# Optimization experiments

Hardware: AMD Instinct MI355X
Metric: run time of the kernel (lower is better)

## Reference

```python
import jax, jax.numpy as jnp
import numpy as np

B, L, H, NHEADS = 32, 1024, 128, 2
HEAD = H // NHEADS
NEG = -2.0**32 + 1.0  # padding value used by the torch module


def setup_inputs() -> dict:
    key = jax.random.key(0)
    ks = jax.random.split(key, 9)
    queries = jax.random.normal(ks[0], (B, L, H), dtype=jnp.float32)
    keys = jax.random.normal(ks[1], (B, L, H), dtype=jnp.float32)
    time_mask = jax.random.bernoulli(ks[2], 0.1, (B, L))
    # causal mask: True above the diagonal (future positions masked)
    attn_mask = jnp.triu(jnp.ones((L, L), dtype=bool), k=1)
    s = 1.0 / np.sqrt(H)
    Qw = jax.random.uniform(ks[3], (H, H), jnp.float32, -s, s)
    Qb = jax.random.uniform(ks[4], (H,), jnp.float32, -s, s)
    Kw = jax.random.uniform(ks[5], (H, H), jnp.float32, -s, s)
    Kb = jax.random.uniform(ks[6], (H,), jnp.float32, -s, s)
    Vw = jax.random.uniform(ks[7], (H, H), jnp.float32, -s, s)
    Vb = jax.random.uniform(ks[8], (H,), jnp.float32, -s, s)
    return {"queries": queries, "keys": keys, "time_mask": time_mask,
            "attn_mask": attn_mask, "Qw": Qw, "Qb": Qb, "Kw": Kw, "Kb": Kb,
            "Vw": Vw, "Vb": Vb}


def reference(queries, keys, time_mask, attn_mask, Qw, Qb, Kw, Kb, Vw, Vb):
    b, l, h = queries.shape
    d = h // NHEADS
    # torch Linear: x @ W.T + b
    Q = queries @ Qw.T + Qb
    K = keys @ Kw.T + Kb
    V = keys @ Vw.T + Vb
    # split heads: torch cat(split(dim=2), dim=0) == (h, B, L, d) layout;
    # equivalent per-head math with (B, h, L, d):
    Qh = Q.reshape(b, l, NHEADS, d).transpose(0, 2, 1, 3)  # bhld
    Kh = K.reshape(b, l, NHEADS, d).transpose(0, 2, 1, 3)
    Vh = V.reshape(b, l, NHEADS, d).transpose(0, 2, 1, 3)
    scores = jnp.einsum('bhqd,bhkd->bhqk', Qh, Kh) / jnp.sqrt(
        jnp.asarray(d, dtype=Qh.dtype))
    # time_mask masks whole query rows; attn_mask is causal over (q, k)
    scores = jnp.where(time_mask[:, None, :, None], NEG, scores)
    scores = jnp.where(attn_mask[None, None, :, :], NEG, scores)
    attn = jax.nn.softmax(scores, axis=-1)  # dropout_rate=0 -> identity
    out = jnp.einsum('bhqk,bhkd->bhqd', attn, Vh)
    return out.transpose(0, 2, 1, 3).reshape(b, l, h)
```

## Files before the change

kernel.cpp:

```cpp
#include <hip/hip_runtime.h>

#define LSEQ 1024
#define DH 64
#define NH 2

typedef __attribute__((ext_vector_type(8))) __bf16 bf16x8;
typedef __attribute__((ext_vector_type(4))) float f32x4;
typedef __attribute__((ext_vector_type(16))) float f32x16;
typedef __attribute__((ext_vector_type(4))) unsigned u32x4;
typedef __attribute__((ext_vector_type(8))) unsigned short ushort8;

__device__ __forceinline__ unsigned short f2bf(float f) {
  unsigned u = __float_as_uint(f);
  u += 0x7FFFu + ((u >> 16) & 1u);
  return (unsigned short)(u >> 16);
}
__device__ __forceinline__ unsigned cvt_pk_bf16(float lo, float hi) {
  unsigned r;
  asm("v_cvt_pk_bf16_f32 %0, %1, %2" : "=v"(r) : "v"(lo), "v"(hi));
  return r;
}
__device__ __forceinline__ void gload16(const void* g, void* l) {
  __builtin_amdgcn_global_load_lds(
      (const __attribute__((address_space(1))) void*)g,
      (__attribute__((address_space(3))) void*)l, 16, 0, 0);
}

#define QSCALE 0.1803368801111601f

__global__ __launch_bounds__(256) void wconv_kernel(
    const float* __restrict__ Qw, const float* __restrict__ Kw,
    const float* __restrict__ Vw, unsigned short* __restrict__ Wbf,
    float* __restrict__ Vmean)
{
  const int t = blockIdx.x * 256 + threadIdx.x;
  if (t < NH * 32 * DH) Vmean[t] = 0.f;
  const int m = t >> 12;
  const float* W = (m == 0) ? Qw : (m == 1) ? Kw : Vw;
  const float4 v = ((const float4*)W)[t & 4095];
  uint2 u;
  u.x = cvt_pk_bf16(v.x, v.y);
  u.y = cvt_pk_bf16(v.z, v.w);
  *(uint2*)&Wbf[t * 4] = u;
}

__global__ __launch_bounds__(256, 3) void proj_kernel(
    const float* __restrict__ queries, const float* __restrict__ keys,
    const unsigned short* __restrict__ Wbf,
    const float* __restrict__ Qb, const float* __restrict__ Kb,
    const float* __restrict__ Vb,
    unsigned short* __restrict__ Qbf, unsigned short* __restrict__ Kbf,
    unsigned short* __restrict__ Vt, float* __restrict__ Vmean)
{
  constexpr int LP = 136;
  __shared__ __align__(16) unsigned short Xs[128 * LP];
  __shared__ __align__(16) unsigned short Wh[8192];

  const int t = threadIdx.x;
  const int lane = t & 63, w = t >> 6;
  const int c = lane & 15, g = lane >> 4;
  const int wrow = w * 32;

  const int mat = blockIdx.x >> 8;
  const int rt  = (blockIdx.x & 255) * 128;
  const float* Xin = (mat == 0) ? queries : keys;
  const char* Wg = (const char*)(Wbf + mat * 16384);

#define WSTAGE_H(h) do {                                                   \
    _Pragma("unroll")                                                      \
    for (int i_ = 0; i_ < 4; ++i_) {                                       \
      const int off_ = t * 16 + i_ * 4096;                   \
      const int lrow_ = off_ >> 7;                             \
      const int lch_ = (off_ >> 4) & 7;                                    \
      gload16(Wg + lrow_ * 256 + (h) * 128 + ((lch_ ^ (lrow_ & 7)) << 4),  \
              (char*)Wh + off_);                                           \
    }                                                                      \
  } while (0)

#define WFRAG_H(ct_, j_) \
  (*(const bf16x8*)&Wh[((ct_) * 16 + c) * 64 + (((j_) ^ (c & 7)) << 3)])

#define XFRAG(half_, kc_) \
  (*(const bf16x8*)&Xs[(wrow + (half_) * 16 + c) * LP + (kc_) * 32 + g * 8])

  WSTAGE_H(0);

  const float4* X4 = (const float4*)(Xin + (size_t)rt * 128);
#pragma unroll
  for (int i = 0; i < 16; ++i) {
    const int e4 = t + i * 256;
    const float4 v = X4[e4];
    const int e = e4 * 4;
    uint2 u;
    u.x = cvt_pk_bf16(v.x, v.y);
    u.y = cvt_pk_bf16(v.z, v.w);
    *(uint2*)&Xs[(e >> 7) * LP + (e & 127)] = u;
  }
  __syncthreads();

  f32x4 acc[2][8];
#pragma unroll
  for (int i = 0; i < 2; ++i)
#pragma unroll
    for (int j = 0; j < 8; ++j) acc[i][j] = (f32x4){0.f, 0.f, 0.f, 0.f};

#pragma unroll
  for (int kc2 = 0; kc2 < 2; ++kc2) {
    const bf16x8 a0 = XFRAG(0, kc2);
    const bf16x8 a1 = XFRAG(1, kc2);
#pragma unroll
    for (int ct = 0; ct < 8; ++ct) {
      const bf16x8 bfr = WFRAG_H(ct, kc2 * 4 + g);
      acc[0][ct] = __builtin_amdgcn_mfma_f32_16x16x32_bf16(a0, bfr, acc[0][ct], 0, 0, 0);
      acc[1][ct] = __builtin_amdgcn_mfma_f32_16x16x32_bf16(a1, bfr, acc[1][ct], 0, 0, 0);
    }
  }
  __syncthreads();
  WSTAGE_H(1);
  __syncthreads();

#pragma unroll
  for (int kc2 = 0; kc2 < 2; ++kc2) {
    const bf16x8 a0 = XFRAG(0, kc2 + 2);
    const bf16x8 a1 = XFRAG(1, kc2 + 2);
#pragma unroll
    for (int ct = 0; ct < 8; ++ct) {
      const bf16x8 bfr = WFRAG_H(ct, kc2 * 4 + g);
      acc[0][ct] = __builtin_amdgcn_mfma_f32_16x16x32_bf16(a0, bfr, acc[0][ct], 0, 0, 0);
      acc[1][ct] = __builtin_amdgcn_mfma_f32_16x16x32_bf16(a1, bfr, acc[1][ct], 0, 0, 0);
    }
  }

  if (mat == 2) {
#pragma unroll
    for (int ct = 0; ct < 8; ++ct) {
      const float bv = Vb[ct * 16 + c];
      float cs = 8.f * bv;
#pragma unroll
      for (int qf = 0; qf < 2; ++qf)
#pragma unroll
        for (int r = 0; r < 4; ++r) cs += acc[qf][ct][r];
      cs += __shfl_xor(cs, 16);
      cs += __shfl_xor(cs, 32);
      if (g == 0) {
        const int col = ct * 16 + c;
        const int bh = (rt >> 10) * NH + (col >> 6);
        atomicAdd(&Vmean[bh * DH + (col & 63)], cs);
      }
    }
    __syncthreads();
#pragma unroll
    for (int qf = 0; qf < 2; ++qf)
#pragma unroll
      for (int ct = 0; ct < 8; ++ct) {
        const float bv = Vb[ct * 16 + c];
        const int col = ct * 16 + c;
        uint2 u;
        u.x = cvt_pk_bf16(acc[qf][ct][0] + bv, acc[qf][ct][1] + bv);
        u.y = cvt_pk_bf16(acc[qf][ct][2] + bv, acc[qf][ct][3] + bv);
        *(uint2*)&Xs[col * LP + wrow + qf * 16 + g * 4] = u;
      }
    __syncthreads();
    const int b = rt >> 10, l0 = rt & 1023;
#pragma unroll
    for (int i = 0; i < 8; ++i) {
      const int e = i * 2048 + t * 8;
      const int col = e >> 7, li = e & 127;
      const ushort8 v8 = *(const ushort8*)&Xs[col * LP + li];
      const int hh = col >> 6, dh = col & 63;
      unsigned short* vp = Vt + ((size_t)(b * NH + hh)) * (DH * LSEQ) +
                           (size_t)dh * LSEQ + l0 + li;
      *(ushort8*)vp = v8;
    }
  } else {
    const float* biasA = mat ? Kb : Qb;
    const float qs = mat ? 1.0f : QSCALE;
    __syncthreads();
#pragma unroll
    for (int qf = 0; qf < 2; ++qf)
#pragma unroll
      for (int ct = 0; ct < 8; ++ct) {
        const float bv = biasA[ct * 16 + c];
#pragma unroll
        for (int r = 0; r < 4; ++r)
          Xs[(wrow + qf * 16 + g * 4 + r) * LP + ct * 16 + c] =
              f2bf((acc[qf][ct][r] + bv) * qs);
      }
    __syncthreads();
    unsigned short* outp = (mat ? Kbf : Qbf) + (size_t)rt * 128;
#pragma unroll
    for (int i = 0; i < 8; ++i) {
      const int e = i * 2048 + t * 8;
      *(ushort8*)&outp[e] = *(const ushort8*)&Xs[(e >> 7) * LP + (e & 127)];
    }
  }
#undef WSTAGE_H
#undef WFRAG_H
#undef XFRAG
}

__global__ __launch_bounds__(128, 2) void attn_kernel(
    const unsigned short* __restrict__ Qbf, const unsigned short* __restrict__ Kbf,
    const unsigned short* __restrict__ Vt, const float* __restrict__ Vmean,
    const int* __restrict__ time_mask, float* __restrict__ out)
{
  __shared__ __align__(16) char smem[33280];

  const int tid = threadIdx.x;
  const int lane = tid & 63, w = tid >> 6;
  const int lq = lane & 31, hi = lane >> 5;
  const int s7 = lq & 7;

  const int wgid = blockIdx.x;
  const int xcd = wgid & 7;
  const int idx = wgid >> 3;
  const int bh  = xcd * 8 + (idx & 7);
  const int qt  = 15 - (idx >> 3);
  const int qbase = qt * 64;
  const int b = bh >> 1, h = bh & 1;

  const unsigned short* Qp = Qbf + ((size_t)b * LSEQ) * 128 + h * 64;
  const char* Kpb = (const char*)(Kbf + ((size_t)b * LSEQ) * 128 + h * 64);
  const char* Vpb = (const char*)(Vt + (size_t)bh * (DH * LSEQ));

  const int nkv = qt + 1;

#define STAGE(tkv, bi) do {                                                   \
    const int kv_ = (tkv) * 64;                                               \
    _Pragma("unroll")                                                         \
    for (int r_ = 0; r_ < 4; ++r_) {                                          \
      const int off_ = tid * 16 + r_ * 2048;                                  \
      const int row_ = off_ >> 7;                                             \
      const int chk_ = (((off_ >> 4) & 7) ^ (row_ & 7)) << 4;                 \
      gload16(Kpb + (size_t)(kv_ + row_) * 256 + chk_,                        \
              (char*)smem + (bi) * 8192 + r_ * 2048 + tid * 16);              \
      gload16(Vpb + (size_t)row_ * 2048 + kv_ * 2 + chk_,                     \
              (char*)smem + 16384 + (bi) * 8192 + r_ * 2048 + tid * 16);      \
    }                                                                         \
  } while (0)

#define PLSWAP(x_, y_) asm("v_permlane32_swap_b32 %0, %1" : "+v"(x_), "+v"(y_))

#define MKPA(pk_, m_, dst_) do {                                              \
    unsigned x0_ = pk_[4*(m_)], x1_ = pk_[4*(m_)+1];                          \
    unsigned y0_ = pk_[4*(m_)+2], y1_ = pk_[4*(m_)+3];                        \
    PLSWAP(x0_, y0_); PLSWAP(x1_, y1_);                                       \
    u32x4 u_ = {x0_, x1_, y0_, y1_};                                          \
    dst_ = *(bf16x8*)&u_;                                                     \
  } while (0)

  bf16x8 qa[4];
#pragma unroll
  for (int kc4 = 0; kc4 < 4; ++kc4)
    qa[kc4] = *(const bf16x8*)&Qp[(qbase + w * 32 + lq) * 128 + kc4 * 16 + hi * 8];

  const __bf16 one = (__bf16)1.0f;
  const bf16x8 vones = {one, one, one, one, one, one, one, one};

  f32x16 acc0 = {}, acc1 = {}, acc5 = {};

  STAGE(0, 0);
  __syncthreads();

  for (int tk = 0; tk < nkv; ++tk) {
    const int cur = tk & 1;
    if (tk + 1 < nkv) STAGE(tk + 1, cur ^ 1);

    const char* Kl = smem + cur * 8192;
    const char* Vl = smem + 16384 + cur * 8192;

    f32x16 s0 = {}, s1 = {};
    __builtin_amdgcn_s_setprio(1);
#pragma unroll
    for (int kc4 = 0; kc4 < 4; ++kc4) {
      const bf16x8 kf = *(const bf16x8*)(Kl + (lq << 7) + (((2 * kc4 + hi) ^ s7) << 4));
      s0 = __builtin_amdgcn_mfma_f32_32x32x16_bf16(kf, qa[kc4], s0, 0, 0, 0);
    }
#pragma unroll
    for (int kc4 = 0; kc4 < 4; ++kc4) {
      const bf16x8 kf = *(const bf16x8*)(Kl + ((32 + lq) << 7) + (((2 * kc4 + hi) ^ s7) << 4));
      s1 = __builtin_amdgcn_mfma_f32_32x32x16_bf16(kf, qa[kc4], s1, 0, 0, 0);
    }
    __builtin_amdgcn_s_setprio(0);

    bf16x8 vf[4][2];
#pragma unroll
    for (int kc4 = 0; kc4 < 4; ++kc4)
#pragma unroll
      for (int dt = 0; dt < 2; ++dt)
        vf[kc4][dt] = *(const bf16x8*)(Vl + ((dt * 32 + lq) << 7) + (((2 * kc4 + hi) ^ s7) << 4));

    const bool diag = (tk == nkv - 1);
    const int kv = tk * 64;
    const int qrow = qbase + w * 32 + lq;
    float p0[16], p1[16];
#pragma unroll
    for (int r = 0; r < 16; ++r) {
      const int krow = (r & 3) + 8 * (r >> 2) + 4 * hi;
      float e0 = __builtin_amdgcn_exp2f(s0[r]);
      float e1 = __builtin_amdgcn_exp2f(s1[r]);
      if (diag) {
        if (kv + krow > qrow)      e0 = 0.f;
        if (kv + 32 + krow > qrow) e1 = 0.f;
      }
      p0[r] = e0; p1[r] = e1;
    }

    unsigned pk0[8], pk1[8];
#pragma unroll
    for (int bb = 0; bb < 4; ++bb) {
      pk0[2*bb]   = cvt_pk_bf16(p0[4*bb],   p0[4*bb+1]);
      pk0[2*bb+1] = cvt_pk_bf16(p0[4*bb+2], p0[4*bb+3]);
      pk1[2*bb]   = cvt_pk_bf16(p1[4*bb],   p1[4*bb+1]);
      pk1[2*bb+1] = cvt_pk_bf16(p1[4*bb+2], p1[4*bb+3]);
    }

    bf16x8 pa;
    __builtin_amdgcn_s_setprio(1);
    MKPA(pk0, 0, pa);
    acc0 = __builtin_amdgcn_mfma_f32_32x32x16_bf16(pa, vf[0][0], acc0, 0, 0, 0);
    acc1 = __builtin_amdgcn_mfma_f32_32x32x16_bf16(pa, vf[0][1], acc1, 0, 0, 0);
    acc5 = __builtin_amdgcn_mfma_f32_32x32x16_bf16(pa, vones,    acc5, 0, 0, 0);
    MKPA(pk0, 1, pa);
    acc0 = __builtin_amdgcn_mfma_f32_32x32x16_bf16(pa, vf[1][0], acc0, 0, 0, 0);
    acc1 = __builtin_amdgcn_mfma_f32_32x32x16_bf16(pa, vf[1][1], acc1, 0, 0, 0);
    acc5 = __builtin_amdgcn_mfma_f32_32x32x16_bf16(pa, vones,    acc5, 0, 0, 0);
    MKPA(pk1, 0, pa);
    acc0 = __builtin_amdgcn_mfma_f32_32x32x16_bf16(pa, vf[2][0], acc0, 0, 0, 0);
    acc1 = __builtin_amdgcn_mfma_f32_32x32x16_bf16(pa, vf[2][1], acc1, 0, 0, 0);
    acc5 = __builtin_amdgcn_mfma_f32_32x32x16_bf16(pa, vones,    acc5, 0, 0, 0);
    MKPA(pk1, 1, pa);
    acc0 = __builtin_amdgcn_mfma_f32_32x32x16_bf16(pa, vf[3][0], acc0, 0, 0, 0);
    acc1 = __builtin_amdgcn_mfma_f32_32x32x16_bf16(pa, vf[3][1], acc1, 0, 0, 0);
    acc5 = __builtin_amdgcn_mfma_f32_32x32x16_bf16(pa, vones,    acc5, 0, 0, 0);
    __builtin_amdgcn_s_setprio(0);

    __syncthreads();
  }

  int* tmx = (int*)(smem + 32768 + w * 128);
  if (hi == 0)
    tmx[lq] = time_mask[b * LSEQ + qbase + w * 32 + lq];
  asm volatile("s_waitcnt lgkmcnt(0)" ::: "memory");
  __builtin_amdgcn_sched_barrier(0);

  const float vmv0 = Vmean[bh * DH + lq]      * (1.0f / 1024.0f);
  const float vmv1 = Vmean[bh * DH + 32 + lq] * (1.0f / 1024.0f);

#pragma unroll
  for (int r = 0; r < 16; ++r) {
    const int qr = (r & 3) + 8 * (r >> 2) + 4 * hi;
    const int tm = tmx[qr];
    const float wv = 1.0f / acc5[r];
    float* orow = out + (size_t)(b * LSEQ + qbase + w * 32 + qr) * (NH * DH) + h * DH;
    orow[lq]      = tm ? vmv0 : acc0[r] * wv;
    orow[32 + lq] = tm ? vmv1 : acc1[r] * wv;
  }
#undef STAGE
#undef PLSWAP
#undef MKPA
}

extern "C" void kernel_launch(void* const* d_in, const int* in_sizes, int n_in,
                              void* d_out, int out_size, void* d_ws, size_t ws_size,
                              hipStream_t stream) {
  const float* queries   = (const float*)d_in[0];
  const float* keys      = (const float*)d_in[1];
  const int*   time_mask = (const int*)d_in[2];
  const float* Qw = (const float*)d_in[4];
  const float* Qb = (const float*)d_in[5];
  const float* Kw = (const float*)d_in[6];
  const float* Kb = (const float*)d_in[7];
  const float* Vw = (const float*)d_in[8];
  const float* Vb = (const float*)d_in[9];
  float* out = (float*)d_out;

  char* ws = (char*)d_ws;
  unsigned short* Wbf   = (unsigned short*)(ws);
  float*          Vmean = (float*)(ws + 98304);
  unsigned short* Qbf   = (unsigned short*)(ws + 114688);
  unsigned short* Kbf   = (unsigned short*)(ws + 8503296);
  unsigned short* Vtp   = (unsigned short*)(ws + 16891904);

  wconv_kernel<<<48, 256, 0, stream>>>(Qw, Kw, Vw, Wbf, Vmean);
  proj_kernel<<<768, 256, 0, stream>>>(queries, keys, Wbf, Qb, Kb, Vb,
                                       Qbf, Kbf, Vtp, Vmean);
  attn_kernel<<<1024, 128, 0, stream>>>(Qbf, Kbf, Vtp, Vmean, time_mask, out);
}
```

Measured before the change: 46.29 us.

## Balance causal attention work by splitting upper query tiles across workgroups with atomics

Restructures the attention grid to balance causal work. Half the workgroups compute the upper-half query tiles over the key tiles from 8 up to the diagonal, then also run a full lower-half query tile. The other half compute the upper-half query tiles over key tiles 0–7 and add partial numerators and row sums into the output with atomics. A new normalization kernel divides the upper-half rows by the accumulated sums and applies the time mask. The weight-conversion kernel gains extra blocks that zero the accumulation targets. This evens out per-workgroup work, at the cost of float atomics, an extra launch, and an extra pass over half the output.

```diff
diff --git a/kernel.cpp b/kernel.cpp
--- a/kernel.cpp
+++ b/kernel.cpp
@@ -31,17 +31,32 @@
 __global__ __launch_bounds__(256) void wconv_kernel(
     const float* __restrict__ Qw, const float* __restrict__ Kw,
     const float* __restrict__ Vw, unsigned short* __restrict__ Wbf,
-    float* __restrict__ Vmean)
+    float* __restrict__ Vmean, float* __restrict__ out,
+    float* __restrict__ lsumbuf)
 {
-  const int t = blockIdx.x * 256 + threadIdx.x;
-  if (t < NH * 32 * DH) Vmean[t] = 0.f;
-  const int m = t >> 12;
-  const float* W = (m == 0) ? Qw : (m == 1) ? Kw : Vw;
-  const float4 v = ((const float4*)W)[t & 4095];
-  uint2 u;
-  u.x = cvt_pk_bf16(v.x, v.y);
-  u.y = cvt_pk_bf16(v.z, v.w);
-  *(uint2*)&Wbf[t * 4] = u;
+  if (blockIdx.x < 48) {
+    const int t = blockIdx.x * 256 + threadIdx.x;
+    if (t < NH * 32 * DH) Vmean[t] = 0.f;
+    const int m = t >> 12;
+    const float* W = (m == 0) ? Qw : (m == 1) ? Kw : Vw;
+    const float4 v = ((const float4*)W)[t & 4095];
+    uint2 u;
+    u.x = cvt_pk_bf16(v.x, v.y);
+    u.y = cvt_pk_bf16(v.z, v.w);
+    *(uint2*)&Wbf[t * 4] = u;
+  } else {
+    const int gid = (blockIdx.x - 48) * 256 + threadIdx.x;
+    const float4 z = {0.f, 0.f, 0.f, 0.f};
+    const int f4 = gid * 2;
+    const int bb = f4 >> 14;
+    const int rem = f4 & 16383;
+    float4* p = (float4*)(out + (size_t)bb * 131072 + 65536) + rem;
+    p[0] = z; p[1] = z;
+    if (gid < 8192) {
+      float4* q = (float4*)lsumbuf + gid * 2;
+      q[0] = z; q[1] = z;
+    }
+  }
 }
 
 __global__ __launch_bounds__(256, 3) void proj_kernel(
@@ -202,7 +217,8 @@
 __global__ __launch_bounds__(128, 2) void attn_kernel(
     const unsigned short* __restrict__ Qbf, const unsigned short* __restrict__ Kbf,
     const unsigned short* __restrict__ Vt, const float* __restrict__ Vmean,
-    const int* __restrict__ time_mask, float* __restrict__ out)
+    const int* __restrict__ time_mask, float* __restrict__ out,
+    float* __restrict__ lsumbuf)
 {
   __shared__ __align__(16) char smem[33280];
 
@@ -215,15 +231,22 @@
   const int xcd = wgid & 7;
   const int idx = wgid >> 3;
   const int bh  = xcd * 8 + (idx & 7);
-  const int qt  = 15 - (idx >> 3);
-  const int qbase = qt * 64;
+  const int ucode = idx >> 3;
   const int b = bh >> 1, h = bh & 1;
 
   const unsigned short* Qp = Qbf + ((size_t)b * LSEQ) * 128 + h * 64;
   const char* Kpb = (const char*)(Kbf + ((size_t)b * LSEQ) * 128 + h * 64);
   const char* Vpb = (const char*)(Vt + (size_t)bh * (DH * LSEQ));
 
-  const int nkv = qt + 1;
+  const int comb = (ucode < 8);
+  int qbase, tkb, tke, tdiag, part;
+  const int nphase = comb ? 2 : 1;
+  if (comb) {
+    const int qt = 8 + ucode;
+    qbase = qt * 64; tkb = 8; tke = qt; tdiag = qt; part = 1;
+  } else {
+    qbase = ucode * 64; tkb = 0; tke = 7; tdiag = -1; part = 1;
+  }
 
 #define STAGE(tkv, bi) do {                                                   \
     const int kv_ = (tkv) * 64;                                               \
@@ -249,116 +272,165 @@
     dst_ = *(bf16x8*)&u_;                                                     \
   } while (0)
 
-  bf16x8 qa[4];
-#pragma unroll
-  for (int kc4 = 0; kc4 < 4; ++kc4)
-    qa[kc4] = *(const bf16x8*)&Qp[(qbase + w * 32 + lq) * 128 + kc4 * 16 + hi * 8];
-
   const __bf16 one = (__bf16)1.0f;
   const bf16x8 vones = {one, one, one, one, one, one, one, one};
 
-  f32x16 acc0 = {}, acc1 = {}, acc5 = {};
-
-  STAGE(0, 0);
-  __syncthreads();
-
-  for (int tk = 0; tk < nkv; ++tk) {
-    const int cur = tk & 1;
-    if (tk + 1 < nkv) STAGE(tk + 1, cur ^ 1);
-
-    const char* Kl = smem + cur * 8192;
-    const char* Vl = smem + 16384 + cur * 8192;
-
-    f32x16 s0 = {}, s1 = {};
-    __builtin_amdgcn_s_setprio(1);
-#pragma unroll
-    for (int kc4 = 0; kc4 < 4; ++kc4) {
-      const bf16x8 kf = *(const bf16x8*)(Kl + (lq << 7) + (((2 * kc4 + hi) ^ s7) << 4));
-      s0 = __builtin_amdgcn_mfma_f32_32x32x16_bf16(kf, qa[kc4], s0, 0, 0, 0);
-    }
-#pragma unroll
-    for (int kc4 = 0; kc4 < 4; ++kc4) {
-      const bf16x8 kf = *(const bf16x8*)(Kl + ((32 + lq) << 7) + (((2 * kc4 + hi) ^ s7) << 4));
-      s1 = __builtin_amdgcn_mfma_f32_32x32x16_bf16(kf, qa[kc4], s1, 0, 0, 0);
-    }
-    __builtin_amdgcn_s_setprio(0);
-
-    bf16x8 vf[4][2];
+  for (int ph = 0; ph < nphase; ++ph) {
+    if (ph == 1) {
+      const int j = 7 - ucode;
+      qbase = j * 64; tkb = 0; tke = j; tdiag = j; part = 0;
+    }
+
+    bf16x8 qa[4];
 #pragma unroll
     for (int kc4 = 0; kc4 < 4; ++kc4)
-#pragma unroll
-      for (int dt = 0; dt < 2; ++dt)
-        vf[kc4][dt] = *(const bf16x8*)(Vl + ((dt * 32 + lq) << 7) + (((2 * kc4 + hi) ^ s7) << 4));
-
-    const bool diag = (tk == nkv - 1);
-    const int kv = tk * 64;
-    const int qrow = qbase + w * 32 + lq;
-    float p0[16], p1[16];
-#pragma unroll
-    for (int r = 0; r < 16; ++r) {
-      const int krow = (r & 3) + 8 * (r >> 2) + 4 * hi;
-      float e0 = __builtin_amdgcn_exp2f(s0[r]);
-      float e1 = __builtin_amdgcn_exp2f(s1[r]);
-      if (diag) {
-        if (kv + krow > qrow)      e0 = 0.f;
-        if (kv + 32 + krow > qrow) e1 = 0.f;
-      }
-      p0[r] = e0; p1[r] = e1;
-    }
-
-    unsigned pk0[8], pk1[8];
-#pragma unroll
-    for (int bb = 0; bb < 4; ++bb) {
-      pk0[2*bb]   = cvt_pk_bf16(p0[4*bb],   p0[4*bb+1]);
-      pk0[2*bb+1] = cvt_pk_bf16(p0[4*bb+2], p0[4*bb+3]);
-      pk1[2*bb]   = cvt_pk_bf16(p1[4*bb],   p1[4*bb+1]);
-      pk1[2*bb+1] = cvt_pk_bf16(p1[4*bb+2], p1[4*bb+3]);
-    }
-
-    bf16x8 pa;
-    __builtin_amdgcn_s_setprio(1);
-    MKPA(pk0, 0, pa);
-    acc0 = __builtin_amdgcn_mfma_f32_32x32x16_bf16(pa, vf[0][0], acc0, 0, 0, 0);
-    acc1 = __builtin_amdgcn_mfma_f32_32x32x16_bf16(pa, vf[0][1], acc1, 0, 0, 0);
-    acc5 = __builtin_amdgcn_mfma_f32_32x32x16_bf16(pa, vones,    acc5, 0, 0, 0);
-    MKPA(pk0, 1, pa);
-    acc0 = __builtin_amdgcn_mfma_f32_32x32x16_bf16(pa, vf[1][0], acc0, 0, 0, 0);
-    acc1 = __builtin_amdgcn_mfma_f32_32x32x16_bf16(pa, vf[1][1], acc1, 0, 0, 0);
-    acc5 = __builtin_amdgcn_mfma_f32_32x32x16_bf16(pa, vones,    acc5, 0, 0, 0);
-    MKPA(pk1, 0, pa);
-    acc0 = __builtin_amdgcn_mfma_f32_32x32x16_bf16(pa, vf[2][0], acc0, 0, 0, 0);
-    acc1 = __builtin_amdgcn_mfma_f32_32x32x16_bf16(pa, vf[2][1], acc1, 0, 0, 0);
-    acc5 = __builtin_amdgcn_mfma_f32_32x32x16_bf16(pa, vones,    acc5, 0, 0, 0);
-    MKPA(pk1, 1, pa);
-    acc0 = __builtin_amdgcn_mfma_f32_32x32x16_bf16(pa, vf[3][0], acc0, 0, 0, 0);
-    acc1 = __builtin_amdgcn_mfma_f32_32x32x16_bf16(pa, vf[3][1], acc1, 0, 0, 0);
-    acc5 = __builtin_amdgcn_mfma_f32_32x32x16_bf16(pa, vones,    acc5, 0, 0, 0);
-    __builtin_amdgcn_s_setprio(0);
-
+      qa[kc4] = *(const bf16x8*)&Qp[(qbase + w * 32 + lq) * 128 + kc4 * 16 + hi * 8];
+
+    f32x16 acc0 = {}, acc1 = {}, acc5 = {};
+
+    STAGE(tkb, tkb & 1);
     __syncthreads();
-  }
-
-  int* tmx = (int*)(smem + 32768 + w * 128);
-  if (hi == 0)
-    tmx[lq] = time_mask[b * LSEQ + qbase + w * 32 + lq];
-  asm volatile("s_waitcnt lgkmcnt(0)" ::: "memory");
-  __builtin_amdgcn_sched_barrier(0);
-
-  const float vmv0 = Vmean[bh * DH + lq]      * (1.0f / 1024.0f);
-  const float vmv1 = Vmean[bh * DH + 32 + lq] * (1.0f / 1024.0f);
-
-#pragma unroll
-  for (int r = 0; r < 16; ++r) {
-    const int qr = (r & 3) + 8 * (r >> 2) + 4 * hi;
-    const int tm = tmx[qr];
-    const float wv = 1.0f / acc5[r];
-    float* orow = out + (size_t)(b * LSEQ + qbase + w * 32 + qr) * (NH * DH) + h * DH;
-    orow[lq]      = tm ? vmv0 : acc0[r] * wv;
-    orow[32 + lq] = tm ? vmv1 : acc1[r] * wv;
+
+    for (int tk = tkb; tk <= tke; ++tk) {
+      const int cur = tk & 1;
+      if (tk < tke) STAGE(tk + 1, cur ^ 1);
+
+      const char* Kl = smem + cur * 8192;
+      const char* Vl = smem + 16384 + cur * 8192;
+
+      f32x16 s0 = {}, s1 = {};
+      __builtin_amdgcn_s_setprio(1);
+#pragma unroll
+      for (int kc4 = 0; kc4 < 4; ++kc4) {
+        const bf16x8 kf = *(const bf16x8*)(Kl + (lq << 7) + (((2 * kc4 + hi) ^ s7) << 4));
+        s0 = __builtin_amdgcn_mfma_f32_32x32x16_bf16(kf, qa[kc4], s0, 0, 0, 0);
+      }
+#pragma unroll
+      for (int kc4 = 0; kc4 < 4; ++kc4) {
+        const bf16x8 kf = *(const bf16x8*)(Kl + ((32 + lq) << 7) + (((2 * kc4 + hi) ^ s7) << 4));
+        s1 = __builtin_amdgcn_mfma_f32_32x32x16_bf16(kf, qa[kc4], s1, 0, 0, 0);
+      }
+      __builtin_amdgcn_s_setprio(0);
+
+      bf16x8 vf[4][2];
+#pragma unroll
+      for (int kc4 = 0; kc4 < 4; ++kc4)
+#pragma unroll
+        for (int dt = 0; dt < 2; ++dt)
+          vf[kc4][dt] = *(const bf16x8*)(Vl + ((dt * 32 + lq) << 7) + (((2 * kc4 + hi) ^ s7) << 4));
+
+      const bool diag = (tk == tdiag);
+      const int kv = tk * 64;
+      const int qrow = qbase + w * 32 + lq;
+      float p0[16], p1[16];
+#pragma unroll
+      for (int r = 0; r < 16; ++r) {
+        const int krow = (r & 3) + 8 * (r >> 2) + 4 * hi;
+        float e0 = __builtin_amdgcn_exp2f(s0[r]);
+        float e1 = __builtin_amdgcn_exp2f(s1[r]);
+        if (diag) {
+          if (kv + krow > qrow)      e0 = 0.f;
+          if (kv + 32 + krow > qrow) e1 = 0.f;
+        }
+        p0[r] = e0; p1[r] = e1;
+      }
+
+      unsigned pk0[8], pk1[8];
+#pragma unroll
+      for (int bb = 0; bb < 4; ++bb) {
+        pk0[2*bb]   = cvt_pk_bf16(p0[4*bb],   p0[4*bb+1]);
+        pk0[2*bb+1] = cvt_pk_bf16(p0[4*bb+2], p0[4*bb+3]);
+        pk1[2*bb]   = cvt_pk_bf16(p1[4*bb],   p1[4*bb+1]);
+        pk1[2*bb+1] = cvt_pk_bf16(p1[4*bb+2], p1[4*bb+3]);
+      }
+
+      bf16x8 pa;
+      __builtin_amdgcn_s_setprio(1);
+      MKPA(pk0, 0, pa);
+      acc0 = __builtin_amdgcn_mfma_f32_32x32x16_bf16(pa, vf[0][0], acc0, 0, 0, 0);
+      acc1 = __builtin_amdgcn_mfma_f32_32x32x16_bf16(pa, vf[0][1], acc1, 0, 0, 0);
+      acc5 = __builtin_amdgcn_mfma_f32_32x32x16_bf16(pa, vones,    acc5, 0, 0, 0);
+      MKPA(pk0, 1, pa);
+      acc0 = __builtin_amdgcn_mfma_f32_32x32x16_bf16(pa, vf[1][0], acc0, 0, 0, 0);
+      acc1 = __builtin_amdgcn_mfma_f32_32x32x16_bf16(pa, vf[1][1], acc1, 0, 0, 0);
+      acc5 = __builtin_amdgcn_mfma_f32_32x32x16_bf16(pa, vones,    acc5, 0, 0, 0);
+      MKPA(pk1, 0, pa);
+      acc0 = __builtin_amdgcn_mfma_f32_32x32x16_bf16(pa, vf[2][0], acc0, 0, 0, 0);
+      acc1 = __builtin_amdgcn_mfma_f32_32x32x16_bf16(pa, vf[2][1], acc1, 0, 0, 0);
+      acc5 = __builtin_amdgcn_mfma_f32_32x32x16_bf16(pa, vones,    acc5, 0, 0, 0);
+      MKPA(pk1, 1, pa);
+      acc0 = __builtin_amdgcn_mfma_f32_32x32x16_bf16(pa, vf[3][0], acc0, 0, 0, 0);
+      acc1 = __builtin_amdgcn_mfma_f32_32x32x16_bf16(pa, vf[3][1], acc1, 0, 0, 0);
+      acc5 = __builtin_amdgcn_mfma_f32_32x32x16_bf16(pa, vones,    acc5, 0, 0, 0);
+      __builtin_amdgcn_s_setprio(0);
+
+      __syncthreads();
+    }
+
+    if (part) {
+#pragma unroll
+      for (int r = 0; r < 16; ++r) {
+        const int qr = (r & 3) + 8 * (r >> 2) + 4 * hi;
+        const int grow = qbase + w * 32 + qr;
+        float* orow = out + (size_t)(b * LSEQ + grow) * (NH * DH) + h * DH;
+        atomicAdd(&orow[lq], acc0[r]);
+        atomicAdd(&orow[32 + lq], acc1[r]);
+        if (lq == 0) atomicAdd(&lsumbuf[bh * LSEQ + grow], acc5[r]);
+      }
+    } else {
+      int* tmx = (int*)(smem + 32768 + w * 128);
+      if (hi == 0)
+        tmx[lq] = time_mask[b * LSEQ + qbase + w * 32 + lq];
+      asm volatile("s_waitcnt lgkmcnt(0)" ::: "memory");
+      __builtin_amdgcn_sched_barrier(0);
+
+      const float vmv0 = Vmean[bh * DH + lq]      * (1.0f / 1024.0f);
+      const float vmv1 = Vmean[bh * DH + 32 + lq] * (1.0f / 1024.0f);
+#pragma unroll
+      for (int r = 0; r < 16; ++r) {
+        const int qr = (r & 3) + 8 * (r >> 2) + 4 * hi;
+        const int tm = tmx[qr];
+        const float wv = 1.0f / acc5[r];
+        float* orow = out + (size_t)(b * LSEQ + qbase + w * 32 + qr) * (NH * DH) + h * DH;
+        orow[lq]      = tm ? vmv0 : acc0[r] * wv;
+        orow[32 + lq] = tm ? vmv1 : acc1[r] * wv;
+      }
+    }
   }
 #undef STAGE
 #undef PLSWAP
 #undef MKPA
+}
+
+__global__ __launch_bounds__(256) void norm_kernel(
+    float* __restrict__ out, const float* __restrict__ lsumbuf,
+    const float* __restrict__ Vmean, const int* __restrict__ time_mask)
+{
+  const int gid = blockIdx.x * 256 + threadIdx.x;
+  const int col8 = gid & 15;
+  const int rb = gid >> 4;
+  const int b = rb >> 9;
+  const int row = 512 + (rb & 511);
+  const int col = col8 * 8;
+  const int h = col >> 6;
+  const int bh = b * NH + h;
+  const int tm = time_mask[b * LSEQ + row];
+  float* p = out + (size_t)(b * LSEQ + row) * (NH * DH) + col;
+  if (tm) {
+    const float* vm = Vmean + bh * DH + (col & 63);
+    float4 o0, o1;
+    o0.x = vm[0] * (1.0f/1024.0f); o0.y = vm[1] * (1.0f/1024.0f);
+    o0.z = vm[2] * (1.0f/1024.0f); o0.w = vm[3] * (1.0f/1024.0f);
+    o1.x = vm[4] * (1.0f/1024.0f); o1.y = vm[5] * (1.0f/1024.0f);
+    o1.z = vm[6] * (1.0f/1024.0f); o1.w = vm[7] * (1.0f/1024.0f);
+    *(float4*)p = o0; *(float4*)(p + 4) = o1;
+  } else {
+    const float inv = 1.0f / lsumbuf[bh * LSEQ + row];
+    float4 a = *(float4*)p, c = *(float4*)(p + 4);
+    a.x *= inv; a.y *= inv; a.z *= inv; a.w *= inv;
+    c.x *= inv; c.y *= inv; c.z *= inv; c.w *= inv;
+    *(float4*)p = a; *(float4*)(p + 4) = c;
+  }
 }
 
 extern "C" void kernel_launch(void* const* d_in, const int* in_sizes, int n_in,
@@ -376,14 +448,17 @@
   float* out = (float*)d_out;
 
   char* ws = (char*)d_ws;
-  unsigned short* Wbf   = (unsigned short*)(ws);
-  float*          Vmean = (float*)(ws + 98304);
-  unsigned short* Qbf   = (unsigned short*)(ws + 114688);
-  unsigned short* Kbf   = (unsigned short*)(ws + 8503296);
-  unsigned short* Vtp   = (unsigned short*)(ws + 16891904);
-
-  wconv_kernel<<<48, 256, 0, stream>>>(Qw, Kw, Vw, Wbf, Vmean);
+  unsigned short* Wbf    = (unsigned short*)(ws);
+  float*          Vmean  = (float*)(ws + 98304);
+  unsigned short* Qbf    = (unsigned short*)(ws + 114688);
+  unsigned short* Kbf    = (unsigned short*)(ws + 8503296);
+  unsigned short* Vtp    = (unsigned short*)(ws + 16891904);
+  float*          lsumbf = (float*)(ws + 25280512);
+
+  wconv_kernel<<<1072, 256, 0, stream>>>(Qw, Kw, Vw, Wbf, Vmean, out, lsumbf);
   proj_kernel<<<768, 256, 0, stream>>>(queries, keys, Wbf, Qb, Kb, Vb,
                                        Qbf, Kbf, Vtp, Vmean);
-  attn_kernel<<<1024, 128, 0, stream>>>(Qbf, Kbf, Vtp, Vmean, time_mask, out);
-}
+  attn_kernel<<<1024, 128, 0, stream>>>(Qbf, Kbf, Vtp, Vmean, time_mask, out,
+                                        lsumbf);
+  norm_kernel<<<1024, 256, 0, stream>>>(out, lsumbf, Vmean, time_mask);
+}
```

Result: slower. 59.72 us (+29.0%).
